# Kernel optimization log

Measured on AMD Instinct MI355X. Metric: run time of the kernel, lower is better.

## Reference

```python
import jax, jax.numpy as jnp
import numpy as np

DIM = 256
HEADS = 8
DIM_HEAD = 64
INNER = HEADS * DIM_HEAD  # 512
B, N = 4, 1024


def setup_inputs() -> dict:
    key = jax.random.key(0)
    ks = jax.random.split(key, 7)
    x = jax.random.normal(ks[0], (B, N, DIM), dtype=jnp.float32)
    attn_bias = jax.random.normal(ks[1], (B, HEADS, N, N), dtype=jnp.float32)
    s = 1.0 / np.sqrt(DIM)
    Wq = jax.random.normal(ks[2], (DIM, INNER), dtype=jnp.float32) * s
    Wkv = jax.random.normal(ks[3], (DIM, 2 * INNER), dtype=jnp.float32) * s
    # to_out initialized to zero in the torch module; use small random so output is non-trivial
    Wo = jax.random.normal(ks[4], (INNER, DIM), dtype=jnp.float32) * (1.0 / np.sqrt(INNER))
    bo = jnp.zeros((DIM,), dtype=jnp.float32)
    # gating initialized weight=0, bias=1 -> sigmoid(1); use small random weight + bias 1
    Wg = jax.random.normal(ks[5], (DIM, INNER), dtype=jnp.float32) * 0.02
    bg = jnp.ones((INNER,), dtype=jnp.float32)
    return {"x": x, "attn_bias": attn_bias, "Wq": Wq, "Wkv": Wkv,
            "Wo": Wo, "bo": bo, "Wg": Wg, "bg": bg}


def reference(x, attn_bias, Wq, Wkv, Wo, bo, Wg, bg):
    b, n, _ = x.shape
    scale = DIM_HEAD ** -0.5
    q = x @ Wq                                    # [b, n, inner]
    kv = x @ Wkv                                  # [b, n, 2*inner]
    k, v = jnp.split(kv, 2, axis=-1)
    def split_heads(t):
        return t.reshape(b, n, HEADS, DIM_HEAD).transpose(0, 2, 1, 3)  # [b,h,n,d]
    q, k, v = split_heads(q) * scale, split_heads(k), split_heads(v)
    dots = jnp.einsum('bhid,bhjd->bhij', q, k) + attn_bias
    # explicit max-subtract then softmax (matches original; numerically identical)
    attn = jax.nn.softmax(dots, axis=-1)
    out = jnp.einsum('bhij,bhjd->bhid', attn, v)  # [b,h,n,d]
    out = out.transpose(0, 2, 1, 3).reshape(b, n, INNER)
    gates = jax.nn.sigmoid(x @ Wg + bg)
    out = out * gates
    return out @ Wo + bo
```

## Files before the change

kernel.cpp:

```cpp
#include <hip/hip_runtime.h>

typedef unsigned short u16;
typedef unsigned int u32;
typedef __attribute__((ext_vector_type(8))) __bf16 bf16x8;
typedef __attribute__((ext_vector_type(4))) float floatx4;
typedef const __attribute__((address_space(1))) unsigned char glob_u8;
typedef __attribute__((address_space(3))) unsigned char lds_u8;

#define DEV __device__ __forceinline__

DEV u16 f2bf(float f) {
  u32 u = __builtin_bit_cast(u32, f);
  u = (u + 0x7fffu + ((u >> 16) & 1u)) >> 16;
  return (u16)u;
}
DEV float bf2f(u16 h) {
  u32 u = ((u32)h) << 16;
  return __builtin_bit_cast(float, u);
}
DEV floatx4 MFMA(bf16x8 a, bf16x8 b, floatx4 c) {
  return __builtin_amdgcn_mfma_f32_16x16x32_bf16(a, b, c, 0, 0, 0);
}

__global__ void convert_k(const float* __restrict__ x, const float* __restrict__ Wq,
                          const float* __restrict__ Wkv, const float* __restrict__ Wg,
                          const float* __restrict__ Wo,
                          u16* __restrict__ xb, u16* __restrict__ WcatT, u16* __restrict__ WoT) {
  int i = blockIdx.x * 256 + threadIdx.x;
  if (i < 1048576) { xb[i] = f2bf(x[i]); return; }
  i -= 1048576;
  if (i < 524288) {
    int n = i >> 8, kk = i & 255;
    float v;
    if (n < 512) v = Wq[kk * 512 + n];
    else if (n < 1536) v = Wkv[kk * 1024 + (n - 512)];
    else v = Wg[kk * 512 + (n - 1536)];
    WcatT[i] = f2bf(v);
    return;
  }
  i -= 524288;
  if (i < 131072) {
    int n = i >> 9, kk = i & 511;
    WoT[i] = f2bf(Wo[kk * 256 + n]);
  }
}

__global__ __launch_bounds__(256, 4) void gemm_qkvg(
    const u16* __restrict__ xb, const u16* __restrict__ WcatT, const float* __restrict__ bg,
    u16* __restrict__ qb, u16* __restrict__ kfrag, u16* __restrict__ vfrag, u16* __restrict__ gb) {
  __shared__ __attribute__((aligned(16))) u16 As[128 * 40];
  __shared__ __attribute__((aligned(16))) u16 Bs[64 * 40];
  const int tid = threadIdx.x;
  const int wave = tid >> 6, lane = tid & 63;
  const int lane15 = lane & 15, quad = lane >> 4;
  const int rm0 = blockIdx.x * 128;
  const int cn0 = blockIdx.y * 64;
  const int wm = (wave & 1) * 64, wn = (wave >> 1) * 32;
  const int rowA = tid >> 1, segA = (tid & 1) * 16;
  const int rowB = tid >> 2, segB = (tid & 3) * 8;
  floatx4 acc[4][2] = {};
  uint4 a0 = *(const uint4*)(xb + (rm0 + rowA) * 256 + segA);
  uint4 a1 = *(const uint4*)(xb + (rm0 + rowA) * 256 + segA + 8);
  uint4 b0 = *(const uint4*)(WcatT + (cn0 + rowB) * 256 + segB);
#pragma unroll 1
  for (int k0 = 0; k0 < 256; k0 += 32) {
    __syncthreads();
    *(uint4*)(As + rowA * 40 + segA) = a0;
    *(uint4*)(As + rowA * 40 + segA + 8) = a1;
    *(uint4*)(Bs + rowB * 40 + segB) = b0;
    __syncthreads();
    if (k0 < 224) {
      a0 = *(const uint4*)(xb + (rm0 + rowA) * 256 + k0 + 32 + segA);
      a1 = *(const uint4*)(xb + (rm0 + rowA) * 256 + k0 + 32 + segA + 8);
      b0 = *(const uint4*)(WcatT + (cn0 + rowB) * 256 + k0 + 32 + segB);
    }
    bf16x8 af[4], bfr[2];
#pragma unroll
    for (int mt = 0; mt < 4; ++mt) af[mt] = *(const bf16x8*)(As + (wm + mt * 16 + lane15) * 40 + quad * 8);
#pragma unroll
    for (int nt = 0; nt < 2; ++nt) bfr[nt] = *(const bf16x8*)(Bs + (wn + nt * 16 + lane15) * 40 + quad * 8);
#pragma unroll
    for (int mt = 0; mt < 4; ++mt)
#pragma unroll
      for (int nt = 0; nt < 2; ++nt)
        acc[mt][nt] = MFMA(af[mt], bfr[nt], acc[mt][nt]);
  }
#pragma unroll
  for (int mt = 0; mt < 4; ++mt)
#pragma unroll
    for (int nt = 0; nt < 2; ++nt)
#pragma unroll
      for (int r = 0; r < 4; ++r) {
        int row = rm0 + wm + mt * 16 + quad * 4 + r;
        int col = cn0 + wn + nt * 16 + lane15;
        float v = acc[mt][nt][r];
        int b = row >> 10, n = row & 1023;
        if (col < 512) {
          int h = col >> 6, d = col & 63;
          qb[((b * 8 + h) * 1024 + n) * 64 + d] = f2bf(v * 0.125f);
        } else if (col < 1024) {
          int c = col - 512, h = c >> 6, d = c & 63;
          int bh2 = b * 8 + h;
          int t = n >> 4, l15 = n & 15;
          int half = d >> 5, qd = (d >> 3) & 3, e = d & 7;
          kfrag[(size_t)bh2 * 65536 + t * 1024 + half * 512 + (qd * 16 + l15) * 8 + e] = f2bf(v);
        } else if (col < 1536) {
          int c = col - 1024, h = c >> 6, d = c & 63;
          int bh2 = b * 8 + h;
          int t64 = n >> 6, ck = (n >> 5) & 1, qd = (n >> 3) & 3, e = n & 7;
          int dt = d >> 4, l15 = d & 15;
          vfrag[(size_t)bh2 * 65536 + t64 * 4096 + dt * 1024 + ck * 512 + (qd * 16 + l15) * 8 + e] = f2bf(v);
        } else {
          int c = col - 1536;
          float g = 1.0f / (1.0f + __expf(-(v + bg[c])));
          gb[row * 512 + c] = f2bf(g);
        }
      }
}

__global__ __launch_bounds__(256, 2) void attn_k(
    const u16* __restrict__ qb, const u16* __restrict__ kfrag, const u16* __restrict__ vfrag,
    const float* __restrict__ bias, const u16* __restrict__ gb, u16* __restrict__ ogb) {
  __shared__ __attribute__((aligned(16))) u16 Kt[2][4096];
  __shared__ __attribute__((aligned(16))) u16 Vt[2][4096];
  __shared__ __attribute__((aligned(16))) float Bt[2][4096];
  __shared__ __attribute__((aligned(16))) u16 Ps[4 * 16 * 72];
  const int tid = threadIdx.x;
  const int wave = tid >> 6, lane = tid & 63;
  const int lane15 = lane & 15, quad = lane >> 4;
  const int bh = blockIdx.x;
  const int q0 = blockIdx.y * 64;

  bf16x8 qf0, qf1;
  {
    const u16* qrow = qb + ((size_t)(bh * 1024 + q0 + wave * 16 + lane15)) * 64 + quad * 8;
    qf0 = *(const bf16x8*)(qrow);
    qf1 = *(const bf16x8*)(qrow + 32);
  }
  bf16x8 ones;
#pragma unroll
  for (int e = 0; e < 8; ++e) ones[e] = __builtin_bit_cast(__bf16, (u16)0x3F80);

  floatx4 oacc[4] = {};
  floatx4 lacc = {};

  u16* Pw = Ps + wave * (16 * 72);
  const u16* kp = kfrag + (size_t)bh * 65536;
  const u16* vp = vfrag + (size_t)bh * 65536;

  auto stage = [&](int kt, int bufi) {
    const int kb0 = kt * 64;
    const u16* kS = kp + kb0 * 64;
    const u16* vS = vp + kb0 * 64;
#pragma unroll
    for (int c = 0; c < 2; ++c) {
      int ch = wave * 2 + c;
      __builtin_amdgcn_global_load_lds((glob_u8*)(kS + ch * 512 + lane * 8),
                                       (lds_u8*)(&Kt[bufi][ch * 512]), 16, 0, 0);
      __builtin_amdgcn_global_load_lds((glob_u8*)(vS + ch * 512 + lane * 8),
                                       (lds_u8*)(&Vt[bufi][ch * 512]), 16, 0, 0);
    }
#pragma unroll
    for (int c = 0; c < 4; ++c) {
      int ch = wave * 4 + c;
      const float* bS = bias + ((size_t)(bh * 1024 + q0 + ch * 4 + quad)) * 1024 + kb0 + lane15 * 4;
      __builtin_amdgcn_global_load_lds((glob_u8*)bS, (lds_u8*)(&Bt[bufi][ch * 256]), 16, 0, 0);
    }
  };

  stage(0, 0);
  __syncthreads();
  int cur = 0;
#pragma unroll 1
  for (int kt = 0; kt < 16; ++kt) {
    if (kt < 15) stage(kt + 1, cur ^ 1);
    const u16* Ktc = Kt[cur];
    const u16* Vtc = Vt[cur];
    const float* Btc = Bt[cur];
    floatx4 s[4];
#pragma unroll
    for (int j = 0; j < 4; ++j) {
      bf16x8 kf0 = *(const bf16x8*)(Ktc + j * 1024 + lane * 8);
      bf16x8 kf1 = *(const bf16x8*)(Ktc + j * 1024 + 512 + lane * 8);
      floatx4 z = {};
      z = MFMA(qf0, kf0, z);
      s[j] = MFMA(qf1, kf1, z);
    }
#pragma unroll
    for (int j = 0; j < 4; ++j)
#pragma unroll
      for (int r = 0; r < 4; ++r)
        s[j][r] = __expf(s[j][r] + Btc[(wave * 16 + quad * 4 + r) * 64 + j * 16 + lane15] - 8.0f);
#pragma unroll
    for (int j = 0; j < 4; ++j)
#pragma unroll
      for (int r = 0; r < 4; ++r)
        Pw[(quad * 4 + r) * 72 + j * 16 + lane15] = f2bf(s[j][r]);
    bf16x8 pf0 = *(const bf16x8*)(Pw + lane15 * 72 + quad * 8);
    bf16x8 pf1 = *(const bf16x8*)(Pw + lane15 * 72 + 32 + quad * 8);

    lacc = MFMA(pf0, ones, lacc);
    lacc = MFMA(pf1, ones, lacc);
#pragma unroll
    for (int dt = 0; dt < 4; ++dt) {
      bf16x8 vf0 = *(const bf16x8*)(Vtc + dt * 1024 + lane * 8);
      bf16x8 vf1 = *(const bf16x8*)(Vtc + dt * 1024 + 512 + lane * 8);
      oacc[dt] = MFMA(pf0, vf0, oacc[dt]);
      oacc[dt] = MFMA(pf1, vf1, oacc[dt]);
    }
    __syncthreads();
    cur ^= 1;
  }

  const int b = bh >> 3, h = bh & 7;
#pragma unroll
  for (int r = 0; r < 4; ++r) {
    int q = q0 + wave * 16 + quad * 4 + r;
    float inv = 1.0f / lacc[r];
    size_t base = ((size_t)(b * 1024 + q)) * 512 + h * 64;
#pragma unroll
    for (int dt = 0; dt < 4; ++dt) {
      size_t gi = base + dt * 16 + lane15;
      ogb[gi] = f2bf(oacc[dt][r] * inv * bf2f(gb[gi]));
    }
  }
}

__global__ __launch_bounds__(256, 4) void gemm_out_k(
    const u16* __restrict__ og, const u16* __restrict__ WoT,
    const float* __restrict__ bo, float* __restrict__ out) {
  __shared__ __attribute__((aligned(16))) u16 As[64 * 40];
  __shared__ __attribute__((aligned(16))) u16 Bs[64 * 40];
  const int tid = threadIdx.x;
  const int wave = tid >> 6, lane = tid & 63;
  const int lane15 = lane & 15, quad = lane >> 4;
  const int rm0 = blockIdx.x * 64;
  const int cn0 = blockIdx.y * 64;
  const int wm = (wave & 1) * 32, wn = (wave >> 1) * 32;
  const int rowA = tid >> 2, segA = (tid & 3) * 8;
  floatx4 acc[2][2] = {};
  uint4 a0 = *(const uint4*)(og + (rm0 + rowA) * 512 + segA);
  uint4 b0 = *(const uint4*)(WoT + (cn0 + rowA) * 512 + segA);
#pragma unroll 1
  for (int k0 = 0; k0 < 512; k0 += 32) {
    __syncthreads();
    *(uint4*)(As + rowA * 40 + segA) = a0;
    *(uint4*)(Bs + rowA * 40 + segA) = b0;
    __syncthreads();
    if (k0 < 480) {
      a0 = *(const uint4*)(og + (rm0 + rowA) * 512 + k0 + 32 + segA);
      b0 = *(const uint4*)(WoT + (cn0 + rowA) * 512 + k0 + 32 + segA);
    }
    bf16x8 af[2], bfr[2];
#pragma unroll
    for (int mt = 0; mt < 2; ++mt) af[mt] = *(const bf16x8*)(As + (wm + mt * 16 + lane15) * 40 + quad * 8);
#pragma unroll
    for (int nt = 0; nt < 2; ++nt) bfr[nt] = *(const bf16x8*)(Bs + (wn + nt * 16 + lane15) * 40 + quad * 8);
#pragma unroll
    for (int mt = 0; mt < 2; ++mt)
#pragma unroll
      for (int nt = 0; nt < 2; ++nt)
        acc[mt][nt] = MFMA(af[mt], bfr[nt], acc[mt][nt]);
  }
#pragma unroll
  for (int nt = 0; nt < 2; ++nt) {
    int col = cn0 + wn + nt * 16 + lane15;
    float bv = bo[col];
#pragma unroll
    for (int mt = 0; mt < 2; ++mt)
#pragma unroll
      for (int r = 0; r < 4; ++r) {
        int row = rm0 + wm + mt * 16 + quad * 4 + r;
        out[(size_t)row * 256 + col] = acc[mt][nt][r] + bv;
      }
  }
}

extern "C" void kernel_launch(void* const* d_in, const int* in_sizes, int n_in,
                              void* d_out, int out_size, void* d_ws, size_t ws_size,
                              hipStream_t stream) {
  const float* x = (const float*)d_in[0];
  const float* bias = (const float*)d_in[1];
  const float* Wq = (const float*)d_in[2];
  const float* Wkv = (const float*)d_in[3];
  const float* Wo = (const float*)d_in[4];
  const float* bo = (const float*)d_in[5];
  const float* Wg = (const float*)d_in[6];
  const float* bg = (const float*)d_in[7];
  float* out = (float*)d_out;
  char* ws = (char*)d_ws;
  u16* xb    = (u16*)(ws);
  u16* WcatT = (u16*)(ws + 2097152);
  u16* WoT   = (u16*)(ws + 3145728);
  u16* qb    = (u16*)(ws + 3407872);
  u16* kfrag = (u16*)(ws + 7602176);
  u16* vfrag = (u16*)(ws + 11796480);
  u16* gb    = (u16*)(ws + 15990784);
  u16* ogb   = (u16*)(ws + 20185088);

  convert_k<<<6656, 256, 0, stream>>>(x, Wq, Wkv, Wg, Wo, xb, WcatT, WoT);
  dim3 g1(32, 32);
  gemm_qkvg<<<g1, 256, 0, stream>>>(xb, WcatT, bg, qb, kfrag, vfrag, gb);
  dim3 g2(32, 16);
  attn_k<<<g2, 256, 0, stream>>>(qb, kfrag, vfrag, bias, gb, ogb);
  dim3 g3(64, 4);
  gemm_out_k<<<g3, 256, 0, stream>>>(ogb, WoT, bo, out);
}
```

Before: 252.6 us.

## Retile projection GEMMs and pad attention bias LDS buffer against bank conflicts

The QKV-gate GEMM moves to 128x128 tiles with a 4x4 MFMA accumulator per wave, halving the grid and raising operand reuse at the cost of more registers and lower occupancy. The output GEMM shrinks to 32-row tiles, doubling its block count so more CUs stay busy on a small problem. The attention kernel's bias tile in LDS gets padding (272-float stride per 4-row chunk) to cut bank conflicts when reading the bias during the softmax exponent step.

```diff
diff --git a/kernel.cpp b/kernel.cpp
--- a/kernel.cpp
+++ b/kernel.cpp
@@ -45,50 +45,52 @@
   }
 }
 
-__global__ __launch_bounds__(256, 4) void gemm_qkvg(
+__global__ __launch_bounds__(256, 2) void gemm_qkvg(
     const u16* __restrict__ xb, const u16* __restrict__ WcatT, const float* __restrict__ bg,
     u16* __restrict__ qb, u16* __restrict__ kfrag, u16* __restrict__ vfrag, u16* __restrict__ gb) {
   __shared__ __attribute__((aligned(16))) u16 As[128 * 40];
-  __shared__ __attribute__((aligned(16))) u16 Bs[64 * 40];
+  __shared__ __attribute__((aligned(16))) u16 Bs[128 * 40];
   const int tid = threadIdx.x;
   const int wave = tid >> 6, lane = tid & 63;
   const int lane15 = lane & 15, quad = lane >> 4;
   const int rm0 = blockIdx.x * 128;
-  const int cn0 = blockIdx.y * 64;
-  const int wm = (wave & 1) * 64, wn = (wave >> 1) * 32;
-  const int rowA = tid >> 1, segA = (tid & 1) * 16;
-  const int rowB = tid >> 2, segB = (tid & 3) * 8;
-  floatx4 acc[4][2] = {};
-  uint4 a0 = *(const uint4*)(xb + (rm0 + rowA) * 256 + segA);
-  uint4 a1 = *(const uint4*)(xb + (rm0 + rowA) * 256 + segA + 8);
-  uint4 b0 = *(const uint4*)(WcatT + (cn0 + rowB) * 256 + segB);
+  const int cn0 = blockIdx.y * 128;
+  const int wm = (wave & 1) * 64, wn = (wave >> 1) * 64;
+  const int rowS = tid >> 1, segS = (tid & 1) * 16;
+  floatx4 acc[4][4] = {};
+  uint4 a0 = *(const uint4*)(xb + (rm0 + rowS) * 256 + segS);
+  uint4 a1 = *(const uint4*)(xb + (rm0 + rowS) * 256 + segS + 8);
+  uint4 b0 = *(const uint4*)(WcatT + (cn0 + rowS) * 256 + segS);
+  uint4 b1 = *(const uint4*)(WcatT + (cn0 + rowS) * 256 + segS + 8);
 #pragma unroll 1
   for (int k0 = 0; k0 < 256; k0 += 32) {
     __syncthreads();
-    *(uint4*)(As + rowA * 40 + segA) = a0;
-    *(uint4*)(As + rowA * 40 + segA + 8) = a1;
-    *(uint4*)(Bs + rowB * 40 + segB) = b0;
+    *(uint4*)(As + rowS * 40 + segS) = a0;
+    *(uint4*)(As + rowS * 40 + segS + 8) = a1;
+    *(uint4*)(Bs + rowS * 40 + segS) = b0;
+    *(uint4*)(Bs + rowS * 40 + segS + 8) = b1;
     __syncthreads();
     if (k0 < 224) {
-      a0 = *(const uint4*)(xb + (rm0 + rowA) * 256 + k0 + 32 + segA);
-      a1 = *(const uint4*)(xb + (rm0 + rowA) * 256 + k0 + 32 + segA + 8);
-      b0 = *(const uint4*)(WcatT + (cn0 + rowB) * 256 + k0 + 32 + segB);
-    }
-    bf16x8 af[4], bfr[2];
+      a0 = *(const uint4*)(xb + (rm0 + rowS) * 256 + k0 + 32 + segS);
+      a1 = *(const uint4*)(xb + (rm0 + rowS) * 256 + k0 + 32 + segS + 8);
+      b0 = *(const uint4*)(WcatT + (cn0 + rowS) * 256 + k0 + 32 + segS);
+      b1 = *(const uint4*)(WcatT + (cn0 + rowS) * 256 + k0 + 32 + segS + 8);
+    }
+    bf16x8 af[4], bfr[4];
 #pragma unroll
     for (int mt = 0; mt < 4; ++mt) af[mt] = *(const bf16x8*)(As + (wm + mt * 16 + lane15) * 40 + quad * 8);
 #pragma unroll
-    for (int nt = 0; nt < 2; ++nt) bfr[nt] = *(const bf16x8*)(Bs + (wn + nt * 16 + lane15) * 40 + quad * 8);
+    for (int nt = 0; nt < 4; ++nt) bfr[nt] = *(const bf16x8*)(Bs + (wn + nt * 16 + lane15) * 40 + quad * 8);
 #pragma unroll
     for (int mt = 0; mt < 4; ++mt)
 #pragma unroll
-      for (int nt = 0; nt < 2; ++nt)
+      for (int nt = 0; nt < 4; ++nt)
         acc[mt][nt] = MFMA(af[mt], bfr[nt], acc[mt][nt]);
   }
 #pragma unroll
   for (int mt = 0; mt < 4; ++mt)
 #pragma unroll
-    for (int nt = 0; nt < 2; ++nt)
+    for (int nt = 0; nt < 4; ++nt)
 #pragma unroll
       for (int r = 0; r < 4; ++r) {
         int row = rm0 + wm + mt * 16 + quad * 4 + r;
@@ -123,7 +125,7 @@
     const float* __restrict__ bias, const u16* __restrict__ gb, u16* __restrict__ ogb) {
   __shared__ __attribute__((aligned(16))) u16 Kt[2][4096];
   __shared__ __attribute__((aligned(16))) u16 Vt[2][4096];
-  __shared__ __attribute__((aligned(16))) float Bt[2][4096];
+  __shared__ __attribute__((aligned(16))) float Btf[2][4352];
   __shared__ __attribute__((aligned(16))) u16 Ps[4 * 16 * 72];
   const int tid = threadIdx.x;
   const int wave = tid >> 6, lane = tid & 63;
@@ -164,7 +166,7 @@
     for (int c = 0; c < 4; ++c) {
       int ch = wave * 4 + c;
       const float* bS = bias + ((size_t)(bh * 1024 + q0 + ch * 4 + quad)) * 1024 + kb0 + lane15 * 4;
-      __builtin_amdgcn_global_load_lds((glob_u8*)bS, (lds_u8*)(&Bt[bufi][ch * 256]), 16, 0, 0);
+      __builtin_amdgcn_global_load_lds((glob_u8*)bS, (lds_u8*)(&Btf[bufi][ch * 272]), 16, 0, 0);
     }
   };
 
@@ -176,7 +178,7 @@
     if (kt < 15) stage(kt + 1, cur ^ 1);
     const u16* Ktc = Kt[cur];
     const u16* Vtc = Vt[cur];
-    const float* Btc = Bt[cur];
+    const float* Btc = Btf[cur];
     floatx4 s[4];
 #pragma unroll
     for (int j = 0; j < 4; ++j) {
@@ -190,7 +192,7 @@
     for (int j = 0; j < 4; ++j)
 #pragma unroll
       for (int r = 0; r < 4; ++r)
-        s[j][r] = __expf(s[j][r] + Btc[(wave * 16 + quad * 4 + r) * 64 + j * 16 + lane15] - 8.0f);
+        s[j][r] = __expf(s[j][r] + Btc[(wave * 4 + quad) * 272 + r * 64 + j * 16 + lane15] - 8.0f);
 #pragma unroll
     for (int j = 0; j < 4; ++j)
 #pragma unroll
@@ -229,50 +231,45 @@
 __global__ __launch_bounds__(256, 4) void gemm_out_k(
     const u16* __restrict__ og, const u16* __restrict__ WoT,
     const float* __restrict__ bo, float* __restrict__ out) {
-  __shared__ __attribute__((aligned(16))) u16 As[64 * 40];
+  __shared__ __attribute__((aligned(16))) u16 As[32 * 40];
   __shared__ __attribute__((aligned(16))) u16 Bs[64 * 40];
   const int tid = threadIdx.x;
   const int wave = tid >> 6, lane = tid & 63;
   const int lane15 = lane & 15, quad = lane >> 4;
-  const int rm0 = blockIdx.x * 64;
+  const int rm0 = blockIdx.x * 32;
   const int cn0 = blockIdx.y * 64;
-  const int wm = (wave & 1) * 32, wn = (wave >> 1) * 32;
-  const int rowA = tid >> 2, segA = (tid & 3) * 8;
-  floatx4 acc[2][2] = {};
-  uint4 a0 = *(const uint4*)(og + (rm0 + rowA) * 512 + segA);
-  uint4 b0 = *(const uint4*)(WoT + (cn0 + rowA) * 512 + segA);
+  const int wm = (wave & 1) * 16, wn = (wave >> 1) * 32;
+  const int rowA = tid >> 3, segA = (tid & 7) * 4;
+  const int rowB = tid >> 2, segB = (tid & 3) * 8;
+  floatx4 acc[2] = {};
+  uint2 a0 = *(const uint2*)(og + (rm0 + rowA) * 512 + segA);
+  uint4 b0 = *(const uint4*)(WoT + (cn0 + rowB) * 512 + segB);
 #pragma unroll 1
   for (int k0 = 0; k0 < 512; k0 += 32) {
     __syncthreads();
-    *(uint4*)(As + rowA * 40 + segA) = a0;
-    *(uint4*)(Bs + rowA * 40 + segA) = b0;
+    *(uint2*)(As + rowA * 40 + segA) = a0;
+    *(uint4*)(Bs + rowB * 40 + segB) = b0;
     __syncthreads();
     if (k0 < 480) {
-      a0 = *(const uint4*)(og + (rm0 + rowA) * 512 + k0 + 32 + segA);
-      b0 = *(const uint4*)(WoT + (cn0 + rowA) * 512 + k0 + 32 + segA);
-    }
-    bf16x8 af[2], bfr[2];
-#pragma unroll
-    for (int mt = 0; mt < 2; ++mt) af[mt] = *(const bf16x8*)(As + (wm + mt * 16 + lane15) * 40 + quad * 8);
+      a0 = *(const uint2*)(og + (rm0 + rowA) * 512 + k0 + 32 + segA);
+      b0 = *(const uint4*)(WoT + (cn0 + rowB) * 512 + k0 + 32 + segB);
+    }
+    bf16x8 af = *(const bf16x8*)(As + (wm + lane15) * 40 + quad * 8);
+    bf16x8 bfr[2];
 #pragma unroll
     for (int nt = 0; nt < 2; ++nt) bfr[nt] = *(const bf16x8*)(Bs + (wn + nt * 16 + lane15) * 40 + quad * 8);
 #pragma unroll
-    for (int mt = 0; mt < 2; ++mt)
-#pragma unroll
-      for (int nt = 0; nt < 2; ++nt)
-        acc[mt][nt] = MFMA(af[mt], bfr[nt], acc[mt][nt]);
+    for (int nt = 0; nt < 2; ++nt) acc[nt] = MFMA(af, bfr[nt], acc[nt]);
   }
 #pragma unroll
   for (int nt = 0; nt < 2; ++nt) {
     int col = cn0 + wn + nt * 16 + lane15;
     float bv = bo[col];
 #pragma unroll
-    for (int mt = 0; mt < 2; ++mt)
-#pragma unroll
-      for (int r = 0; r < 4; ++r) {
-        int row = rm0 + wm + mt * 16 + quad * 4 + r;
-        out[(size_t)row * 256 + col] = acc[mt][nt][r] + bv;
-      }
+    for (int r = 0; r < 4; ++r) {
+      int row = rm0 + wm + quad * 4 + r;
+      out[(size_t)row * 256 + col] = acc[nt][r] + bv;
+    }
   }
 }
 
@@ -299,10 +296,10 @@
   u16* ogb   = (u16*)(ws + 20185088);
 
   convert_k<<<6656, 256, 0, stream>>>(x, Wq, Wkv, Wg, Wo, xb, WcatT, WoT);
-  dim3 g1(32, 32);
+  dim3 g1(32, 16);
   gemm_qkvg<<<g1, 256, 0, stream>>>(xb, WcatT, bg, qb, kfrag, vfrag, gb);
   dim3 g2(32, 16);
   attn_k<<<g2, 256, 0, stream>>>(qb, kfrag, vfrag, bias, gb, ogb);
-  dim3 g3(64, 4);
+  dim3 g3(128, 4);
   gemm_out_k<<<g3, 256, 0, stream>>>(ogb, WoT, bo, out);
 }
```

Measured after the change: 258.9 us. +2.5%, slower.
